# Optimization experiments

Hardware: AMD Instinct MI355X
Metric: run time of the kernel (lower is better)

## Reference

```python
import jax, jax.numpy as jnp
import numpy as np
import math

B, S, D, H = 4, 2048, 1024, 16
HD = D // H  # head_dim = 64


def _rope_tables(max_len, half_dim, theta=10000.0):
    inv_freq = 1.0 / (theta ** (jnp.arange(0, half_dim, dtype=jnp.float32) / half_dim))
    ang = jnp.arange(max_len, dtype=jnp.float32)[:, None] * inv_freq[None, :]  # [max_len, half_dim]
    return jnp.cos(ang), jnp.sin(ang)


def _apply_rope(x, cos, sin):
    # x: [B, H, S, HD]; cos/sin: [S, HD/2]
    x1, x2 = x[..., ::2], x[..., 1::2]
    # matches torch.cat([x1*cos - x2*sin, x1*sin + x2*cos], dim=-1)
    return jnp.concatenate([x1 * cos - x2 * sin, x1 * sin + x2 * cos], axis=-1)


def setup_inputs() -> dict:
    key = jax.random.key(0)
    kx, kq, ko = jax.random.split(key, 3)
    x = jax.random.normal(kx, (B, S, D), dtype=jnp.float32)
    Wqkv = jax.random.normal(kq, (D, 3 * D), dtype=jnp.float32) / math.sqrt(D)
    Wout = jax.random.normal(ko, (D, D), dtype=jnp.float32) / math.sqrt(D)
    cos, sin = _rope_tables(S, HD // 2)
    # causal additive mask, per-batch as in module signature [B, S, S]
    causal = jnp.where(jnp.tril(jnp.ones((S, S), dtype=bool)), 0.0, -1e9).astype(jnp.float32)
    mask = jnp.broadcast_to(causal, (B, S, S))
    return {"x": x, "cos": cos, "sin": sin, "mask": mask, "Wqkv": Wqkv, "Wout": Wout}


def reference(x, cos, sin, mask, Wqkv, Wout):
    b, s, d = x.shape
    qkv = x @ Wqkv  # [B, S, 3D]
    q, k, v = jnp.split(qkv, 3, axis=-1)
    def to_heads(t):
        return t.reshape(b, s, H, HD).transpose(0, 2, 1, 3)  # [B, H, S, HD]
    q, k, v = to_heads(q), to_heads(k), to_heads(v)
    q = _apply_rope(q, cos[:s], sin[:s])
    k = _apply_rope(k, cos[:s], sin[:s])
    scores = jnp.einsum("bhqd,bhkd->bhqk", q, k) / math.sqrt(HD)
    attn = jax.nn.softmax(scores + mask[:, None, :, :], axis=-1)
    out = jnp.einsum("bhqk,bhkd->bhqd", attn, v)  # [B, H, S, HD]
    out = out.transpose(0, 2, 1, 3).reshape(b, s, d)
    return out @ Wout
```

## Files before the change

kernel.cpp:

```cpp
#include <hip/hip_runtime.h>
#include <hip/hip_bf16.h>
#include <stdint.h>

#define B_   4
#define S_   2048
#define D_   1024
#define H_   16
#define HD_  64
#define BH_  (B_*H_)
#define MROWS (B_*S_)

typedef short  short8  __attribute__((ext_vector_type(8)));
typedef float  floatx4 __attribute__((ext_vector_type(4)));

__device__ __forceinline__ ushort f2bf(float f) {
    union { float f; uint32_t u; } v; v.f = f;
    uint32_t u = v.u;
    return (ushort)((u + 0x7FFFu + ((u >> 16) & 1u)) >> 16);
}
__device__ __forceinline__ float bf2f(ushort b) {
    union { uint32_t u; float f; } v; v.u = ((uint32_t)b) << 16;
    return v.f;
}

__device__ __forceinline__ void gl_lds16(const ushort* g, ushort* l) {
    __builtin_amdgcn_global_load_lds(
        (const __attribute__((address_space(1))) unsigned int*)g,
        (__attribute__((address_space(3))) unsigned int*)l,
        16, 0, 0);
}

__global__ void k_f32_to_bf16(const float* __restrict__ in, ushort* __restrict__ out, int n) {
    int i = (blockIdx.x * blockDim.x + threadIdx.x) * 4;
    if (i + 3 < n) {
        float4 f = *(const float4*)(in + i);
        ushort4 o; o.x = f2bf(f.x); o.y = f2bf(f.y); o.z = f2bf(f.z); o.w = f2bf(f.w);
        *(ushort4*)(out + i) = o;
    }
}

__global__ void k_transpose_to_bf16(const float* __restrict__ in, ushort* __restrict__ out,
                                    int R, int C) {
    __shared__ float tile[32][33];
    int bx = blockIdx.x * 32;
    int by = blockIdx.y * 32;
    int tx = threadIdx.x;
    int ty = threadIdx.y;
    #pragma unroll
    for (int j = 0; j < 32; j += 8)
        tile[ty + j][tx] = in[(size_t)(by + ty + j) * C + bx + tx];
    __syncthreads();
    #pragma unroll
    for (int j = 0; j < 32; j += 8)
        out[(size_t)(bx + ty + j) * R + by + tx] = f2bf(tile[tx][ty + j]);
}

__global__ void k_vtrans(const ushort* __restrict__ Vb, ushort* __restrict__ VbT) {
    __shared__ __align__(16) ushort t[64 * 72];
    int bh = blockIdx.x >> 5;
    int s0 = (blockIdx.x & 31) * 64;
    int tid = threadIdx.x;
    int ss = tid >> 2, c0 = (tid & 3) * 16;
    size_t base = (size_t)bh * S_ * HD_;
    *(uint4*)&t[ss * 72 + c0]     = *(const uint4*)&Vb[base + (size_t)(s0 + ss) * HD_ + c0];
    *(uint4*)&t[ss * 72 + c0 + 8] = *(const uint4*)&Vb[base + (size_t)(s0 + ss) * HD_ + c0 + 8];
    __syncthreads();
    int hd = tid >> 2, q0 = (tid & 3) * 16;
    ushort tmp[16];
    #pragma unroll
    for (int e = 0; e < 16; e++) tmp[e] = t[(q0 + e) * 72 + hd];
    size_t obase = (size_t)bh * HD_ * S_ + (size_t)hd * S_ + s0 + q0;
    *(uint4*)&VbT[obase]     = *(const uint4*)&tmp[0];
    *(uint4*)&VbT[obase + 8] = *(const uint4*)&tmp[8];
}

#define BM 128
#define BN 128
#define BK 32
#define LDT 32

template<int EPI>
__global__ __launch_bounds__(256)
void k_gemm(const ushort* __restrict__ A, const ushort* __restrict__ Bt,
            float* __restrict__ outF,
            ushort* __restrict__ q_out, ushort* __restrict__ k_out, ushort* __restrict__ v_out,
            int M, int N, int K) {
    __shared__ __align__(16) ushort As[BM * LDT];
    __shared__ __align__(16) ushort Bs[BN * LDT];
    int tid  = threadIdx.x;
    int lane = tid & 63;
    int wave = tid >> 6;
    int quad = lane >> 4;
    int l16  = lane & 15;
    int bm = blockIdx.y * BM;
    int bn = blockIdx.x * BN;
    int wm = (wave >> 1) * 64;
    int wn = (wave & 1) * 64;

    floatx4 acc[4][4] = {};

    for (int k0 = 0; k0 < K; k0 += BK) {
        __syncthreads();
        #pragma unroll
        for (int p = 0; p < 2; p++) {
            int c   = p * 256 + tid;
            int row = c >> 2;
            int kc  = (c & 3) << 3;
            gl_lds16(&A[(size_t)(bm + row) * K + k0 + kc],  &As[c * 8]);
            gl_lds16(&Bt[(size_t)(bn + row) * K + k0 + kc], &Bs[c * 8]);
        }
        __syncthreads();
        short8 af[4], bf[4];
        #pragma unroll
        for (int mt = 0; mt < 4; mt++)
            af[mt] = *(const short8*)&As[(wm + mt * 16 + l16) * LDT + quad * 8];
        #pragma unroll
        for (int nt = 0; nt < 4; nt++)
            bf[nt] = *(const short8*)&Bs[(wn + nt * 16 + l16) * LDT + quad * 8];
        #pragma unroll
        for (int mt = 0; mt < 4; mt++)
            #pragma unroll
            for (int nt = 0; nt < 4; nt++)
                acc[mt][nt] = __builtin_amdgcn_mfma_f32_16x16x32_bf16(af[mt], bf[nt], acc[mt][nt], 0, 0, 0);
    }

    #pragma unroll
    for (int mt = 0; mt < 4; mt++)
        #pragma unroll
        for (int nt = 0; nt < 4; nt++)
            #pragma unroll
            for (int r = 0; r < 4; r++) {
                int row = bm + wm + mt * 16 + quad * 4 + r;
                int col = bn + wn + nt * 16 + l16;
                float v = acc[mt][nt][r];
                if (EPI == 0) {
                    int which = col >> 10;
                    int rem   = col & 1023;
                    int h  = rem >> 6, hd = rem & 63;
                    int b  = row >> 11, s  = row & 2047;
                    size_t idx = ((size_t)(b * H_ + h) * S_ + s) * HD_ + hd;
                    ushort bv = f2bf(v);
                    ushort* dst = (which == 0) ? q_out : (which == 1) ? k_out : v_out;
                    dst[idx] = bv;
                } else {
                    outF[(size_t)row * N + col] = v;
                }
            }
}

__global__ void k_rope(ushort* __restrict__ Q, ushort* __restrict__ Kv,
                       const float* __restrict__ cosT, const float* __restrict__ sinT) {
    int wid  = (blockIdx.x * 256 + threadIdx.x) >> 6;
    int lane = threadIdx.x & 63;
    int s  = wid & (S_ - 1);
    int bh = wid >> 11;
    int i  = lane & 31;
    float c  = cosT[s * 32 + i];
    float sn = sinT[s * 32 + i];
    size_t base = ((size_t)bh * S_ + s) * HD_;

    float x1 = bf2f(Q[base + 2 * i]), x2 = bf2f(Q[base + 2 * i + 1]);
    float o  = (lane < 32) ? (x1 * c - x2 * sn) : (x1 * sn + x2 * c);
    Q[base + lane] = f2bf(o);

    x1 = bf2f(Kv[base + 2 * i]); x2 = bf2f(Kv[base + 2 * i + 1]);
    o  = (lane < 32) ? (x1 * c - x2 * sn) : (x1 * sn + x2 * c);
    Kv[base + lane] = f2bf(o);
}

__global__ __launch_bounds__(256, 4)
void k_attn(const ushort* __restrict__ Q, const ushort* __restrict__ K,
            const ushort* __restrict__ VT, ushort* __restrict__ O) {
    __shared__ __align__(16) ushort Ksp[2][64 * 32];
    __shared__ __align__(16) ushort Vtp[2][64 * 32];
    __shared__ __align__(16) ushort Pst[4][32 * 72];

    int tid  = threadIdx.x;
    int lane = tid & 63;
    int wave = tid >> 6;
    int quad = lane >> 4;
    int l16  = lane & 15;

    int bh   = blockIdx.x & 63;
    int qblk = 15 - (blockIdx.x >> 6);
    int qb0  = qblk * 128;
    size_t hbase = (size_t)bh * S_ * HD_;
    size_t vbase = (size_t)bh * HD_ * S_;

    int mrow[2] = { qb0 + wave * 16, qb0 + 64 + wave * 16 };

    short8 qf[2][2];
    #pragma unroll
    for (int m = 0; m < 2; m++)
        #pragma unroll
        for (int h = 0; h < 2; h++)
            qf[m][h] = *(const short8*)&Q[hbase + (size_t)(mrow[m] + l16) * HD_ + quad * 8 + h * 32];

    floatx4 acc[2][4] = {};
    float lsum[2][4] = {};

    int crow = tid >> 2;
    int coff = (tid & 3) * 8;

    int nk = 2 * qblk + 2;
    for (int kb = 0; kb < nk; kb++) {
        int k0 = kb * 64;
        __syncthreads();
        #pragma unroll
        for (int h = 0; h < 2; h++)
            gl_lds16(&K[hbase + (size_t)(k0 + crow) * HD_ + h * 32 + coff], &Ksp[h][tid * 8]);
        #pragma unroll
        for (int k2 = 0; k2 < 2; k2++)
            gl_lds16(&VT[vbase + (size_t)crow * S_ + k0 + k2 * 32 + coff], &Vtp[k2][tid * 8]);
        __syncthreads();

        bool act0 = (k0 <= mrow[0] + 15);
        bool act1 = (k0 <= mrow[1] + 15);

        #pragma unroll
        for (int m = 0; m < 2; m++) {
            if (!(m == 0 ? act0 : act1)) continue;
            floatx4 sc[4] = {};
            #pragma unroll
            for (int kt = 0; kt < 4; kt++)
                #pragma unroll
                for (int h = 0; h < 2; h++) {
                    short8 kf = *(const short8*)&Ksp[h][(kt * 16 + l16) * 32 + quad * 8];
                    sc[kt] = __builtin_amdgcn_mfma_f32_16x16x32_bf16(qf[m][h], kf, sc[kt], 0, 0, 0);
                }
            bool needMask = (k0 + 63 > mrow[m]);
            #pragma unroll
            for (int kt = 0; kt < 4; kt++)
                #pragma unroll
                for (int r = 0; r < 4; r++) {
                    float p = __expf(sc[kt][r] * 0.125f);
                    if (needMask) {
                        int qr = mrow[m] + quad * 4 + r;
                        int kc = k0 + kt * 16 + l16;
                        if (kc > qr) p = 0.0f;
                    }
                    lsum[m][r] += p;
                    Pst[wave][(m * 16 + quad * 4 + r) * 72 + kt * 16 + l16] = f2bf(p);
                }
        }

        short8 vb[4][2];
        #pragma unroll
        for (int nt = 0; nt < 4; nt++)
            #pragma unroll
            for (int k2 = 0; k2 < 2; k2++)
                vb[nt][k2] = *(const short8*)&Vtp[k2][(nt * 16 + l16) * 32 + quad * 8];

        #pragma unroll
        for (int m = 0; m < 2; m++) {
            if (!(m == 0 ? act0 : act1)) continue;
            #pragma unroll
            for (int k2 = 0; k2 < 2; k2++) {
                short8 pa = *(const short8*)&Pst[wave][(m * 16 + l16) * 72 + k2 * 32 + quad * 8];
                #pragma unroll
                for (int nt = 0; nt < 4; nt++)
                    acc[m][nt] = __builtin_amdgcn_mfma_f32_16x16x32_bf16(pa, vb[nt][k2], acc[m][nt], 0, 0, 0);
            }
        }
    }

    #pragma unroll
    for (int off = 1; off < 16; off <<= 1)
        #pragma unroll
        for (int m = 0; m < 2; m++)
            #pragma unroll
            for (int r = 0; r < 4; r++)
                lsum[m][r] += __shfl_xor(lsum[m][r], off);

    int b = bh >> 4, h = bh & 15;
    #pragma unroll
    for (int m = 0; m < 2; m++)
        #pragma unroll
        for (int r = 0; r < 4; r++) {
            float inv = 1.0f / lsum[m][r];
            int qr = mrow[m] + quad * 4 + r;
            #pragma unroll
            for (int nt = 0; nt < 4; nt++)
                O[((size_t)(b * S_ + qr)) * D_ + h * HD_ + nt * 16 + l16] = f2bf(acc[m][nt][r] * inv);
        }
}

extern "C" void kernel_launch(void* const* d_in, const int* in_sizes, int n_in,
                              void* d_out, int out_size, void* d_ws, size_t ws_size,
                              hipStream_t stream) {
    const float* x    = (const float*)d_in[0];
    const float* cosT = (const float*)d_in[1];
    const float* sinT = (const float*)d_in[2];
    const float* Wqkv = (const float*)d_in[4];
    const float* Wout = (const float*)d_in[5];
    float* out = (float*)d_out;

    ushort* ws = (ushort*)d_ws;
    ushort* Xbf    = ws;
    ushort* WqkvT  = Xbf    + (size_t)MROWS * D_;
    ushort* WoutT  = WqkvT  + (size_t)3 * D_ * D_;
    ushort* Qb     = WoutT  + (size_t)D_ * D_;
    ushort* Kb     = Qb     + (size_t)BH_ * S_ * HD_;
    ushort* Vb     = Kb     + (size_t)BH_ * S_ * HD_;
    ushort* VbT    = Vb     + (size_t)BH_ * S_ * HD_;
    ushort* AO     = Xbf;

    k_f32_to_bf16<<<(MROWS * D_) / 1024, 256, 0, stream>>>(x, Xbf, MROWS * D_);
    k_transpose_to_bf16<<<dim3(3 * D_ / 32, D_ / 32), dim3(32, 8), 0, stream>>>(Wqkv, WqkvT, D_, 3 * D_);
    k_transpose_to_bf16<<<dim3(D_ / 32, D_ / 32), dim3(32, 8), 0, stream>>>(Wout, WoutT, D_, D_);
    k_gemm<0><<<dim3(3 * D_ / BN, MROWS / BM), 256, 0, stream>>>(Xbf, WqkvT, nullptr, Qb, Kb, Vb,
                                                                 MROWS, 3 * D_, D_);
    k_rope<<<(BH_ * S_ * 64) / 256, 256, 0, stream>>>(Qb, Kb, cosT, sinT);
    k_vtrans<<<BH_ * 32, 256, 0, stream>>>(Vb, VbT);
    k_attn<<<1024, 256, 0, stream>>>(Qb, Kb, VbT, AO);
    k_gemm<1><<<dim3(D_ / BN, MROWS / BM), 256, 0, stream>>>(AO, WoutT, out, nullptr, nullptr, nullptr,
                                                             MROWS, D_, D_);
}
```

Baseline: 332.8 us.

## Transpose QK MFMA operands so P rows pack into vectorized LDS stores

Swaps the A/B operands of the QK^T MFMA so each lane holds four consecutive key columns for a single query row. This lets P be packed into bf16 pairs with perm and written with one 8-byte LDS store instead of four scalar stores, and reduces each row sum to two cross-quad shuffles shared through LDS. It also folds the 1/sqrt(d) scale into Q during RoPE, hoists the K fragment loads out of the m loop, loads RoPE pairs as 32-bit words, and reorders the PV loop to cut live V registers. The bf16 rounding of P becomes round-half-up rather than round-to-nearest-even, and Lw is read without a barrier, which is safe only because each wave reads its own slot.

```diff
diff --git a/kernel.cpp b/kernel.cpp
--- a/kernel.cpp
+++ b/kernel.cpp
@@ -21,6 +21,12 @@
 __device__ __forceinline__ float bf2f(ushort b) {
     union { uint32_t u; float f; } v; v.u = ((uint32_t)b) << 16;
     return v.f;
+}
+__device__ __forceinline__ float u2f(uint32_t u) {
+    union { uint32_t u; float f; } v; v.u = u; return v.f;
+}
+__device__ __forceinline__ uint32_t f2u(float f) {
+    union { float f; uint32_t u; } v; v.f = f; return v.u;
 }
 
 __device__ __forceinline__ void gl_lds16(const ushort* g, ushort* l) {
@@ -159,11 +165,13 @@
     float sn = sinT[s * 32 + i];
     size_t base = ((size_t)bh * S_ + s) * HD_;
 
-    float x1 = bf2f(Q[base + 2 * i]), x2 = bf2f(Q[base + 2 * i + 1]);
+    uint32_t uq = *(const uint32_t*)&Q[base + 2 * i];
+    float x1 = u2f(uq << 16), x2 = u2f(uq & 0xFFFF0000u);
     float o  = (lane < 32) ? (x1 * c - x2 * sn) : (x1 * sn + x2 * c);
-    Q[base + lane] = f2bf(o);
-
-    x1 = bf2f(Kv[base + 2 * i]); x2 = bf2f(Kv[base + 2 * i + 1]);
+    Q[base + lane] = f2bf(o * 0.125f);
+
+    uint32_t uk = *(const uint32_t*)&Kv[base + 2 * i];
+    x1 = u2f(uk << 16); x2 = u2f(uk & 0xFFFF0000u);
     o  = (lane < 32) ? (x1 * c - x2 * sn) : (x1 * sn + x2 * c);
     Kv[base + lane] = f2bf(o);
 }
@@ -174,6 +182,7 @@
     __shared__ __align__(16) ushort Ksp[2][64 * 32];
     __shared__ __align__(16) ushort Vtp[2][64 * 32];
     __shared__ __align__(16) ushort Pst[4][32 * 72];
+    __shared__ float Lw[4][32];
 
     int tid  = threadIdx.x;
     int lane = tid & 63;
@@ -197,7 +206,7 @@
             qf[m][h] = *(const short8*)&Q[hbase + (size_t)(mrow[m] + l16) * HD_ + quad * 8 + h * 32];
 
     floatx4 acc[2][4] = {};
-    float lsum[2][4] = {};
+    float lsum[2] = {0.0f, 0.0f};
 
     int crow = tid >> 2;
     int coff = (tid & 3) * 8;
@@ -214,70 +223,76 @@
             gl_lds16(&VT[vbase + (size_t)crow * S_ + k0 + k2 * 32 + coff], &Vtp[k2][tid * 8]);
         __syncthreads();
 
-        bool act0 = (k0 <= mrow[0] + 15);
-        bool act1 = (k0 <= mrow[1] + 15);
+        bool act[2] = { k0 <= mrow[0] + 15, k0 <= mrow[1] + 15 };
+
+        short8 kf[4][2];
+        #pragma unroll
+        for (int kt = 0; kt < 4; kt++)
+            #pragma unroll
+            for (int h = 0; h < 2; h++)
+                kf[kt][h] = *(const short8*)&Ksp[h][(kt * 16 + l16) * 32 + quad * 8];
 
         #pragma unroll
         for (int m = 0; m < 2; m++) {
-            if (!(m == 0 ? act0 : act1)) continue;
+            if (!act[m]) continue;
             floatx4 sc[4] = {};
             #pragma unroll
             for (int kt = 0; kt < 4; kt++)
                 #pragma unroll
-                for (int h = 0; h < 2; h++) {
-                    short8 kf = *(const short8*)&Ksp[h][(kt * 16 + l16) * 32 + quad * 8];
-                    sc[kt] = __builtin_amdgcn_mfma_f32_16x16x32_bf16(qf[m][h], kf, sc[kt], 0, 0, 0);
-                }
+                for (int h = 0; h < 2; h++)
+                    sc[kt] = __builtin_amdgcn_mfma_f32_16x16x32_bf16(kf[kt][h], qf[m][h], sc[kt], 0, 0, 0);
             bool needMask = (k0 + 63 > mrow[m]);
-            #pragma unroll
-            for (int kt = 0; kt < 4; kt++)
+            int qr = mrow[m] + l16;
+            #pragma unroll
+            for (int kt = 0; kt < 4; kt++) {
+                float p[4];
                 #pragma unroll
                 for (int r = 0; r < 4; r++) {
-                    float p = __expf(sc[kt][r] * 0.125f);
+                    float v = __expf(sc[kt][r]);
                     if (needMask) {
-                        int qr = mrow[m] + quad * 4 + r;
-                        int kc = k0 + kt * 16 + l16;
-                        if (kc > qr) p = 0.0f;
+                        int kc = k0 + kt * 16 + quad * 4 + r;
+                        if (kc > qr) v = 0.0f;
                     }
-                    lsum[m][r] += p;
-                    Pst[wave][(m * 16 + quad * 4 + r) * 72 + kt * 16 + l16] = f2bf(p);
+                    p[r] = v;
                 }
+                lsum[m] += (p[0] + p[1]) + (p[2] + p[3]);
+                uint2 pk;
+                pk.x = __builtin_amdgcn_perm(f2u(p[1]) + 0x8000u, f2u(p[0]) + 0x8000u, 0x07060302u);
+                pk.y = __builtin_amdgcn_perm(f2u(p[3]) + 0x8000u, f2u(p[2]) + 0x8000u, 0x07060302u);
+                *(uint2*)&Pst[wave][(m * 16 + l16) * 72 + kt * 16 + quad * 4] = pk;
+            }
         }
 
-        short8 vb[4][2];
-        #pragma unroll
-        for (int nt = 0; nt < 4; nt++)
-            #pragma unroll
-            for (int k2 = 0; k2 < 2; k2++)
-                vb[nt][k2] = *(const short8*)&Vtp[k2][(nt * 16 + l16) * 32 + quad * 8];
-
-        #pragma unroll
-        for (int m = 0; m < 2; m++) {
-            if (!(m == 0 ? act0 : act1)) continue;
-            #pragma unroll
-            for (int k2 = 0; k2 < 2; k2++) {
+        #pragma unroll
+        for (int k2 = 0; k2 < 2; k2++) {
+            short8 vb[4];
+            #pragma unroll
+            for (int nt = 0; nt < 4; nt++)
+                vb[nt] = *(const short8*)&Vtp[k2][(nt * 16 + l16) * 32 + quad * 8];
+            #pragma unroll
+            for (int m = 0; m < 2; m++) {
+                if (!act[m]) continue;
                 short8 pa = *(const short8*)&Pst[wave][(m * 16 + l16) * 72 + k2 * 32 + quad * 8];
                 #pragma unroll
                 for (int nt = 0; nt < 4; nt++)
-                    acc[m][nt] = __builtin_amdgcn_mfma_f32_16x16x32_bf16(pa, vb[nt][k2], acc[m][nt], 0, 0, 0);
+                    acc[m][nt] = __builtin_amdgcn_mfma_f32_16x16x32_bf16(pa, vb[nt], acc[m][nt], 0, 0, 0);
             }
         }
     }
 
     #pragma unroll
-    for (int off = 1; off < 16; off <<= 1)
-        #pragma unroll
-        for (int m = 0; m < 2; m++)
-            #pragma unroll
-            for (int r = 0; r < 4; r++)
-                lsum[m][r] += __shfl_xor(lsum[m][r], off);
+    for (int m = 0; m < 2; m++) {
+        lsum[m] += __shfl_xor(lsum[m], 16);
+        lsum[m] += __shfl_xor(lsum[m], 32);
+        if (quad == 0) Lw[wave][m * 16 + l16] = lsum[m];
+    }
 
     int b = bh >> 4, h = bh & 15;
     #pragma unroll
     for (int m = 0; m < 2; m++)
         #pragma unroll
         for (int r = 0; r < 4; r++) {
-            float inv = 1.0f / lsum[m][r];
+            float inv = 1.0f / Lw[wave][m * 16 + quad * 4 + r];
             int qr = mrow[m] + quad * 4 + r;
             #pragma unroll
             for (int nt = 0; nt < 4; nt++)
```

Result: slower. 346.0 us (+4.0%).
